# Optimization experiments

Measured on AMD Instinct MI355X. Metric: run time of the kernel, lower is better.

The kernel has to match this reference:

```python
import jax, jax.numpy as jnp
import numpy as np

SMOOTH_WEIGHT = 0.2
SMOOTH_THRESHOLD = 0.2
POS_WEIGHT = 2.0  # class_weight=[2.0]


def setup_inputs() -> dict:
    key = jax.random.key(0)
    k1, k2, k3, k4 = jax.random.split(key, 4)
    B, T, R = 2048, 16, 2048
    return {
        "predictions": jax.random.normal(k1, (B, T, 1), dtype=jnp.float32),
        "region_scores": jax.random.normal(k2, (B, T, R, 1), dtype=jnp.float32),
        "targets": jax.random.randint(k3, (B, T), 0, 2, dtype=jnp.int32),
        "valid_mask": jax.random.randint(k4, (B, T), 0, 2, dtype=jnp.int32),
    }


def reference(predictions, region_scores, targets, valid_mask):
    # predictions: [B, T, 1]; region_scores: [B, T, R, 1]
    y = targets.astype(jnp.float32)[..., None]          # [B, T, 1]
    vm = valid_mask.astype(jnp.float32)[..., None]      # [B, T, 1]

    # BCEWithLogits with pos_weight, reduction='none'
    bce = -(POS_WEIGHT * y * jax.nn.log_sigmoid(predictions)
            + (1.0 - y) * jax.nn.log_sigmoid(-predictions))
    class_loss = (bce * vm).sum() / jnp.maximum(vm.sum(), 1e-8)

    # Smoothness penalty on consecutive region scores where both steps valid
    pair_valid = (vm[:, 1:, 0] > 0.5) & (vm[:, :-1, 0] > 0.5)  # [B, T-1]
    diff = region_scores[:, 1:] - region_scores[:, :-1]        # [B, T-1, R, 1]
    pen = jnp.square(jax.nn.relu(jnp.abs(diff) - SMOOTH_THRESHOLD))
    pen = pen.mean(axis=(2, 3))                                # [B, T-1] mean over regions

    count = pair_valid.sum(axis=0)                             # [T-1] valid samples per step
    pv = pair_valid.astype(pen.dtype)
    step_loss = (pen * pv).sum(axis=0) / jnp.maximum(count, 1) # 0 where count==0
    num_steps = (count > 0).sum()
    smooth_loss = jnp.where(num_steps > 0,
                            step_loss.sum() / jnp.maximum(num_steps, 1),
                            0.0)

    total_loss = class_loss + SMOOTH_WEIGHT * smooth_loss
    return total_loss
```

## Files before the change

kernel.cpp:

```cpp
#include <hip/hip_runtime.h>

#define BB 2048
#define TT 16
#define RR 2048
#define NPAIR (TT - 1)

__device__ __forceinline__ float log_sigmoid(float x) {
    return fminf(x, 0.0f) - log1pf(expf(-fabsf(x)));
}

__global__ void class_loss_kernel(const float* __restrict__ pred,
                                  const int* __restrict__ targets,
                                  const int* __restrict__ vm,
                                  float* __restrict__ ws) {
    int tid = blockIdx.x * blockDim.x + threadIdx.x;
    int stride = gridDim.x * blockDim.x;
    float bce_sum = 0.f, vm_sum = 0.f;
    for (int i = tid; i < BB * TT; i += stride) {
        float x = pred[i];
        float y = (float)targets[i];
        float v = (float)vm[i];
        float bce = -(2.0f * y * log_sigmoid(x) + (1.0f - y) * log_sigmoid(-x));
        bce_sum += bce * v;
        vm_sum += v;
    }
    #pragma unroll
    for (int off = 32; off; off >>= 1) {
        bce_sum += __shfl_down(bce_sum, off);
        vm_sum  += __shfl_down(vm_sum, off);
    }
    __shared__ float s_b[8], s_v[8];
    int lane = threadIdx.x & 63, wave = threadIdx.x >> 6;
    if (lane == 0) { s_b[wave] = bce_sum; s_v[wave] = vm_sum; }
    __syncthreads();
    if (threadIdx.x == 0) {
        float b = 0.f, v = 0.f;
        int nw = blockDim.x >> 6;
        for (int w = 0; w < nw; ++w) { b += s_b[w]; v += s_v[w]; }
        atomicAdd(&ws[0], b);
        atomicAdd(&ws[1], v);
    }
}

__global__ __launch_bounds__(512)
void smooth_kernel(const float* __restrict__ rs,
                   const int* __restrict__ vm,
                   float* __restrict__ S,
                   int* __restrict__ counts) {
    int b = blockIdx.x;
    __shared__ int s_vm[TT];
    if (threadIdx.x < TT) s_vm[threadIdx.x] = vm[b * TT + threadIdx.x];
    __syncthreads();

    bool pv[NPAIR];
    #pragma unroll
    for (int p = 0; p < NPAIR; ++p) pv[p] = (s_vm[p] != 0) && (s_vm[p + 1] != 0);

    const float4* base = (const float4*)(rs + (size_t)b * TT * RR);
    const int r4 = threadIdx.x;

    float acc[NPAIR];
    #pragma unroll
    for (int p = 0; p < NPAIR; ++p) acc[p] = 0.f;

    float4 prev = make_float4(0.f, 0.f, 0.f, 0.f);
    #pragma unroll
    for (int t = 0; t < TT; ++t) {
        bool need = ((t > 0) && pv[t - 1]) || ((t < NPAIR) && pv[t]);
        float4 cur = prev;
        if (need) cur = base[t * (RR / 4) + r4];
        if (t > 0 && pv[t - 1]) {
            float dx = fmaxf(fabsf(cur.x - prev.x) - 0.2f, 0.f);
            float dy = fmaxf(fabsf(cur.y - prev.y) - 0.2f, 0.f);
            float dz = fmaxf(fabsf(cur.z - prev.z) - 0.2f, 0.f);
            float dw = fmaxf(fabsf(cur.w - prev.w) - 0.2f, 0.f);
            acc[t - 1] += dx * dx + dy * dy + dz * dz + dw * dw;
        }
        prev = cur;
    }

    __shared__ float s_acc[8][NPAIR];
    int lane = threadIdx.x & 63, wave = threadIdx.x >> 6;
    #pragma unroll
    for (int p = 0; p < NPAIR; ++p) {
        if (pv[p]) {
            float v = acc[p];
            #pragma unroll
            for (int off = 32; off; off >>= 1) v += __shfl_down(v, off);
            if (lane == 0) s_acc[wave][p] = v;
        }
    }
    __syncthreads();
    if (threadIdx.x < NPAIR) {
        int p = threadIdx.x;
        if (pv[p]) {
            float s = 0.f;
            #pragma unroll
            for (int w = 0; w < 8; ++w) s += s_acc[w][p];
            atomicAdd(&S[p], s);
            atomicAdd(&counts[p], 1);
        }
    }
}

__global__ void finalize_kernel(const float* __restrict__ ws,
                                const int* __restrict__ counts,
                                float* __restrict__ out) {
    if (threadIdx.x != 0 || blockIdx.x != 0) return;
    float class_loss = ws[0] / fmaxf(ws[1], 1e-8f);
    float step_sum = 0.f;
    int num_steps = 0;
    for (int p = 0; p < NPAIR; ++p) {
        int c = counts[p];
        float pen_sum = ws[2 + p] / (float)RR;
        float step = pen_sum / (float)(c > 0 ? c : 1);
        step_sum += step;
        if (c > 0) ++num_steps;
    }
    float smooth = (num_steps > 0) ? (step_sum / (float)num_steps) : 0.f;
    out[0] = class_loss + 0.2f * smooth;
}

extern "C" void kernel_launch(void* const* d_in, const int* in_sizes, int n_in,
                              void* d_out, int out_size, void* d_ws, size_t ws_size,
                              hipStream_t stream) {
    const float* pred    = (const float*)d_in[0];
    const float* rs      = (const float*)d_in[1];
    const int*   targets = (const int*)d_in[2];
    const int*   vmask   = (const int*)d_in[3];
    float* out = (float*)d_out;
    float* ws  = (float*)d_ws;
    hipMemsetAsync(d_ws, 0, 32 * sizeof(float), stream);

    class_loss_kernel<<<32, 256, 0, stream>>>(pred, targets, vmask, ws);
    smooth_kernel<<<BB, 512, 0, stream>>>(rs, vmask, ws + 2, (int*)(ws + 17));
    finalize_kernel<<<1, 64, 0, stream>>>(ws, (int*)(ws + 17), out);
}
```

Measured before the change: 339.5 us.

## Split smooth kernel across two time halves and batch loads up front

Each batch row is now handled by two blocks, one for time steps 0-8 and one for 8-15. Each block issues all of its float4 loads into a register array before doing any compute, which raises memory-level parallelism and doubles the grid. The cost is that the boundary step 8 is read twice and there are more atomics. The class-loss grid is also doubled.

```diff
diff --git a/kernel.cpp b/kernel.cpp
--- a/kernel.cpp
+++ b/kernel.cpp
@@ -47,42 +47,52 @@
                    const int* __restrict__ vm,
                    float* __restrict__ S,
                    int* __restrict__ counts) {
-    int b = blockIdx.x;
+    const int b = blockIdx.x >> 1;
+    const int h = blockIdx.x & 1;
+    const int t0 = h * 8;
+    const int np = h ? 7 : 8;
+    const int ns = h ? 8 : 9;
+
     __shared__ int s_vm[TT];
     if (threadIdx.x < TT) s_vm[threadIdx.x] = vm[b * TT + threadIdx.x];
     __syncthreads();
 
-    bool pv[NPAIR];
+    bool pv[8];
     #pragma unroll
-    for (int p = 0; p < NPAIR; ++p) pv[p] = (s_vm[p] != 0) && (s_vm[p + 1] != 0);
+    for (int i = 0; i < 8; ++i) {
+        int gp = t0 + i;
+        pv[i] = (i < np) && (s_vm[gp] != 0) && (s_vm[gp + 1] != 0);
+    }
 
     const float4* base = (const float4*)(rs + (size_t)b * TT * RR);
     const int r4 = threadIdx.x;
 
-    float acc[NPAIR];
+    float4 sl[9];
     #pragma unroll
-    for (int p = 0; p < NPAIR; ++p) acc[p] = 0.f;
-
-    float4 prev = make_float4(0.f, 0.f, 0.f, 0.f);
-    #pragma unroll
-    for (int t = 0; t < TT; ++t) {
-        bool need = ((t > 0) && pv[t - 1]) || ((t < NPAIR) && pv[t]);
-        float4 cur = prev;
-        if (need) cur = base[t * (RR / 4) + r4];
-        if (t > 0 && pv[t - 1]) {
-            float dx = fmaxf(fabsf(cur.x - prev.x) - 0.2f, 0.f);
-            float dy = fmaxf(fabsf(cur.y - prev.y) - 0.2f, 0.f);
-            float dz = fmaxf(fabsf(cur.z - prev.z) - 0.2f, 0.f);
-            float dw = fmaxf(fabsf(cur.w - prev.w) - 0.2f, 0.f);
-            acc[t - 1] += dx * dx + dy * dy + dz * dz + dw * dw;
-        }
-        prev = cur;
+    for (int i = 0; i < 9; ++i) {
+        bool need = (i < ns) && (((i > 0) && pv[i - 1]) || pv[i < 8 ? i : 7] && (i < 8));
+        if (i == 8) need = (i < ns) && pv[7];
+        if (need) sl[i] = base[(t0 + i) * (RR / 4) + r4];
+        else      sl[i] = make_float4(0.f, 0.f, 0.f, 0.f);
     }
 
-    __shared__ float s_acc[8][NPAIR];
+    float acc[8];
+    #pragma unroll
+    for (int p = 0; p < 8; ++p) {
+        acc[p] = 0.f;
+        if (pv[p]) {
+            float dx = fmaxf(fabsf(sl[p + 1].x - sl[p].x) - 0.2f, 0.f);
+            float dy = fmaxf(fabsf(sl[p + 1].y - sl[p].y) - 0.2f, 0.f);
+            float dz = fmaxf(fabsf(sl[p + 1].z - sl[p].z) - 0.2f, 0.f);
+            float dw = fmaxf(fabsf(sl[p + 1].w - sl[p].w) - 0.2f, 0.f);
+            acc[p] = dx * dx + dy * dy + dz * dz + dw * dw;
+        }
+    }
+
+    __shared__ float s_acc[8][8];
     int lane = threadIdx.x & 63, wave = threadIdx.x >> 6;
     #pragma unroll
-    for (int p = 0; p < NPAIR; ++p) {
+    for (int p = 0; p < 8; ++p) {
         if (pv[p]) {
             float v = acc[p];
             #pragma unroll
@@ -91,14 +101,14 @@
         }
     }
     __syncthreads();
-    if (threadIdx.x < NPAIR) {
+    if (threadIdx.x < 8) {
         int p = threadIdx.x;
         if (pv[p]) {
             float s = 0.f;
             #pragma unroll
             for (int w = 0; w < 8; ++w) s += s_acc[w][p];
-            atomicAdd(&S[p], s);
-            atomicAdd(&counts[p], 1);
+            atomicAdd(&S[t0 + p], s);
+            atomicAdd(&counts[t0 + p], 1);
         }
     }
 }
@@ -132,7 +142,7 @@
     float* ws  = (float*)d_ws;
     hipMemsetAsync(d_ws, 0, 32 * sizeof(float), stream);
 
-    class_loss_kernel<<<32, 256, 0, stream>>>(pred, targets, vmask, ws);
-    smooth_kernel<<<BB, 512, 0, stream>>>(rs, vmask, ws + 2, (int*)(ws + 17));
+    class_loss_kernel<<<64, 256, 0, stream>>>(pred, targets, vmask, ws);
+    smooth_kernel<<<BB * 2, 512, 0, stream>>>(rs, vmask, ws + 2, (int*)(ws + 17));
     finalize_kernel<<<1, 64, 0, stream>>>(ws, (int*)(ws + 17), out);
 }
```

Measured after the change: 351.5 us. 3.5% more time.
